# Kernel tuning notes

Hardware: AMD Instinct MI355X
Metric: run time of the kernel (lower is better)

## Reference

```python
import jax, jax.numpy as jnp
import numpy as np

B, CIN, H, W = 32, 64, 128, 128
HID, OUT, E, S, R = 64, 64, 8, 2, 16
TOP_K = 2
TEMP = 2.0
BN_EPS = 1e-5


def setup_inputs() -> dict:
    key = jax.random.key(0)
    ks = jax.random.split(key, 16)
    sc = lambda fan: 1.0 / np.sqrt(fan)
    h2 = 2 * HID
    return {
        "x": jax.random.normal(ks[0], (B, CIN, H, W), jnp.float32),
        "fe_w": jax.random.normal(ks[1], (HID, CIN), jnp.float32) * sc(CIN),
        "fe_b": jnp.zeros((HID,), jnp.float32),
        "s_w": jax.random.normal(ks[2], (S, OUT, HID), jnp.float32) * sc(HID),
        "s_b": jnp.zeros((S, OUT), jnp.float32),
        "e_w": jax.random.normal(ks[3], (E, OUT, HID), jnp.float32) * sc(HID),
        "e_b": jnp.zeros((E, OUT), jnp.float32),
        "g1_w": jax.random.normal(ks[4], (h2, HID), jnp.float32) * sc(HID),
        "g1_b": jnp.zeros((h2,), jnp.float32),
        "bn1_g": jnp.ones((h2,), jnp.float32),
        "bn1_b": jnp.zeros((h2,), jnp.float32),
        "ca1_w": jax.random.normal(ks[5], (h2 // R, h2), jnp.float32) * sc(h2),
        "ca1_b": jnp.zeros((h2 // R,), jnp.float32),
        "ca2_w": jax.random.normal(ks[6], (h2, h2 // R), jnp.float32) * sc(h2 // R),
        "ca2_b": jnp.zeros((h2,), jnp.float32),
        "g2_w": jax.random.normal(ks[7], (HID, h2), jnp.float32) * sc(h2),
        "g2_b": jnp.zeros((HID,), jnp.float32),
        "bn2_g": jnp.ones((HID,), jnp.float32),
        "bn2_b": jnp.zeros((HID,), jnp.float32),
        "g3_w": jax.random.normal(ks[8], (E, HID), jnp.float32) * sc(HID),
        "g3_b": jnp.zeros((E,), jnp.float32),
    }


def _gelu(v):
    return jax.nn.gelu(v, approximate=False)


def _bn_eval(v, g, b):
    # BatchNorm eval mode with running_mean=0, running_var=1
    return v * (g / np.sqrt(1.0 + BN_EPS)) + b


def reference(x, fe_w, fe_b, s_w, s_b, e_w, e_b, g1_w, g1_b, bn1_g, bn1_b,
              ca1_w, ca1_b, ca2_w, ca2_b, g2_w, g2_b, bn2_g, bn2_b, g3_w, g3_b):
    # feature extractor: 1x1 conv + GELU
    features = _gelu(jnp.einsum('bchw,oc->bohw', x, fe_w) + fe_b[None, :, None, None])

    # shared experts: mean of S expert outputs (sum / S)
    shared = _gelu(jnp.einsum('bchw,soc->bsohw', features, s_w)
                   + s_b[None, :, :, None, None]).mean(axis=1)

    # gating on globally pooled features [B, HID]
    gf = features.mean(axis=(2, 3))
    h1 = _gelu(_bn_eval(gf @ g1_w.T + g1_b, bn1_g, bn1_b))  # [B, 2*HID]
    # ChannelAttention on 1x1 spatial: avg_pool == max_pool == identity
    att = _gelu(h1 @ ca1_w.T + ca1_b) @ ca2_w.T + ca2_b
    h1 = h1 * jax.nn.sigmoid(att + att)  # avg_out + max_out are identical
    hh = _gelu(_bn_eval(h1 @ g2_w.T + g2_b, bn2_g, bn2_b))  # [B, HID]
    scores = hh @ g3_w.T + g3_b  # [B, E]

    top_vals, top_idx = jax.lax.top_k(scores, TOP_K)
    top_w = jax.nn.softmax(top_vals / TEMP, axis=1)  # [B, TOP_K]
    # dense per-(sample, expert) weights
    dense_w = jnp.zeros((x.shape[0], E), scores.dtype).at[
        jnp.arange(x.shape[0])[:, None], top_idx].add(top_w)

    # all experts on full batch, then weighted accumulate (matches original loop)
    eo = _gelu(jnp.einsum('bchw,eoc->beohw', features, e_w)
               + e_b[None, :, :, None, None])  # [B, E, OUT, H, W]
    routed = jnp.einsum('beohw,be->bohw', eo, dense_w)

    return shared + routed
```

## Files before the change

kernel.cpp:

```cpp
#include <hip/hip_runtime.h>
#include <hip/hip_bf16.h>
#include <stdint.h>

#define HW 16384
#define BATCH 32

typedef __bf16 bf16_t;
typedef bf16_t bf16x8 __attribute__((ext_vector_type(8)));
typedef float f32x4 __attribute__((ext_vector_type(4)));

__device__ __forceinline__ float gelu_f(float x) {
    float t = x * fmaf(x * x, 0.044715f, 1.0f);
    float e = __builtin_amdgcn_exp2f(-2.3022083f * t);
    return x * __builtin_amdgcn_rcpf(1.0f + e);
}

__device__ __forceinline__ uint32_t pk2(float a, float b) {
    union { bf16_t h[2]; uint32_t u; } z;
    z.h[0] = (bf16_t)a; z.h[1] = (bf16_t)b;
    return z.u;
}

__global__ __launch_bounds__(64)
void k0_conv(const float* __restrict__ fe_w, const float* __restrict__ s_w,
             const float* __restrict__ e_w, bf16_t* __restrict__ wbf) {
    int blk = blockIdx.x;
    int m = blk >> 3;
    int ot = (blk >> 1) & 3;
    int kh = blk & 1;
    int lane = threadIdx.x;
    int r16 = lane & 15, g = lane >> 4;

    const float* W;
    if (m == 0) W = fe_w;
    else if (m <= 2) W = s_w + (size_t)(m - 1) * 4096;
    else W = e_w + (size_t)(m - 3) * 4096;

    const float* src = W + (ot * 16 + r16) * 64 + kh * 32 + g * 8;
    float4 lo = ((const float4*)src)[0];
    float4 hi = ((const float4*)src)[1];
    bf16x8 r;
    r[0] = (bf16_t)lo.x; r[1] = (bf16_t)lo.y; r[2] = (bf16_t)lo.z; r[3] = (bf16_t)lo.w;
    r[4] = (bf16_t)hi.x; r[5] = (bf16_t)hi.y; r[6] = (bf16_t)hi.z; r[7] = (bf16_t)hi.w;
    *(bf16x8*)(wbf + (size_t)blk * 512 + lane * 8) = r;
}

__global__ __launch_bounds__(256, 4)
void k1_feat(const float* __restrict__ x, const bf16_t* __restrict__ wbf,
             const float* __restrict__ fe_b, bf16_t* __restrict__ feat,
             float* __restrict__ gf_sum) {
    __shared__ bf16_t xs[64 * 258];
    __shared__ float gf4[4][64];

    int tid = threadIdx.x;
    int lane = tid & 63;
    int wid = tid >> 6;
    int r16 = lane & 15;
    int g = lane >> 4;
    int b = blockIdx.x >> 6;
    int stripe = blockIdx.x & 63;
    int p0 = stripe * 256;

    bf16x8 A[4][2];
    f32x4 bias[4];
#pragma unroll
    for (int ot = 0; ot < 4; ++ot) {
#pragma unroll
        for (int kh = 0; kh < 2; ++kh)
            A[ot][kh] = *(const bf16x8*)(wbf + (size_t)((0 * 4 + ot) * 2 + kh) * 512 + lane * 8);
#pragma unroll
        for (int r = 0; r < 4; ++r) bias[ot][r] = fe_b[ot * 16 + g * 4 + r];
    }

    uint32_t* xsw = (uint32_t*)xs;
#pragma unroll
    for (int i = 0; i < 16; ++i) {
        int lid = i * 256 + tid;
        int c = lid >> 6;
        int pc = lid & 63;
        float4 v = ((const float4*)(x + (size_t)(b * 64 + c) * HW + p0))[pc];
        int widx = c * 129 + pc * 2;
        xsw[widx] = pk2(v.x, v.y);
        xsw[widx + 1] = pk2(v.z, v.w);
    }
    __syncthreads();

    float gfp[4][4] = {};
    bf16_t* featb = feat + (size_t)b * HW * 64;

#pragma unroll
    for (int t = 0; t < 4; ++t) {
        int pl = (wid * 4 + t) * 16 + r16;
        bf16x8 B0, B1;
#pragma unroll
        for (int j = 0; j < 8; ++j) {
            B0[j] = xs[(g * 8 + j) * 258 + pl];
            B1[j] = xs[(32 + g * 8 + j) * 258 + pl];
        }
        int pg = p0 + pl;
#pragma unroll
        for (int ot = 0; ot < 4; ++ot) {
            f32x4 y = {0.f, 0.f, 0.f, 0.f};
            y = __builtin_amdgcn_mfma_f32_16x16x32_bf16(A[ot][0], B0, y, 0, 0, 0);
            y = __builtin_amdgcn_mfma_f32_16x16x32_bf16(A[ot][1], B1, y, 0, 0, 0);
            float vr[4];
#pragma unroll
            for (int r = 0; r < 4; ++r) {
                float v = gelu_f(y[r] + bias[ot][r]);
                gfp[ot][r] += v;
                vr[r] = v;
            }
            uint2 st;
            st.x = pk2(vr[0], vr[1]);
            st.y = pk2(vr[2], vr[3]);
            *(uint2*)(featb + (size_t)pg * 64 + ot * 16 + g * 4) = st;
        }
    }

#pragma unroll
    for (int ot = 0; ot < 4; ++ot) {
#pragma unroll
        for (int r = 0; r < 4; ++r) {
            float v = gfp[ot][r];
            v += __shfl_xor(v, 1);
            v += __shfl_xor(v, 2);
            v += __shfl_xor(v, 4);
            v += __shfl_xor(v, 8);
            if (r16 == 0) gf4[wid][ot * 16 + g * 4 + r] = v;
        }
    }
    __syncthreads();
    if (tid < 64) {
        float s = gf4[0][tid] + gf4[1][tid] + gf4[2][tid] + gf4[3][tid];
        atomicAdd(gf_sum + b * 64 + tid, s);
    }
}

__global__ __launch_bounds__(256)
void k2_gate(const float* __restrict__ gf_sum,
             const float* __restrict__ g1_w, const float* __restrict__ g1_b,
             const float* __restrict__ bn1_g, const float* __restrict__ bn1_b,
             const float* __restrict__ ca1_w, const float* __restrict__ ca1_b,
             const float* __restrict__ ca2_w, const float* __restrict__ ca2_b,
             const float* __restrict__ g2_w, const float* __restrict__ g2_b,
             const float* __restrict__ bn2_g, const float* __restrict__ bn2_b,
             const float* __restrict__ g3_w, const float* __restrict__ g3_b,
             int* __restrict__ gidx, float* __restrict__ gw) {
    __shared__ float gf[32 * 64];
    __shared__ float h1[32 * 128];
    __shared__ float a1[32 * 8];
    __shared__ float hh[32 * 64];
    __shared__ float sc[32 * 8];
    const float R1 = 0.99999500003749969f;
    int tid = threadIdx.x;

    for (int i = tid; i < 2048; i += 256) gf[i] = gf_sum[i] * (1.0f / 16384.0f);
    __syncthreads();

    for (int e = tid; e < 4096; e += 256) {
        int b = e >> 7, j = e & 127;
        float s = g1_b[j];
        for (int c = 0; c < 64; ++c) s += gf[b * 64 + c] * g1_w[j * 64 + c];
        s = s * (bn1_g[j] * R1) + bn1_b[j];
        h1[e] = gelu_f(s);
    }
    __syncthreads();
    {
        int b = tid >> 3, j = tid & 7;
        float s = ca1_b[j];
        for (int c = 0; c < 128; ++c) s += h1[b * 128 + c] * ca1_w[j * 128 + c];
        a1[tid] = gelu_f(s);
    }
    __syncthreads();
    for (int e = tid; e < 4096; e += 256) {
        int b = e >> 7, j = e & 127;
        float s = ca2_b[j];
        for (int r = 0; r < 8; ++r) s += a1[b * 8 + r] * ca2_w[j * 8 + r];
        float e2 = __builtin_amdgcn_exp2f(-2.8853901f * s);
        h1[e] = h1[e] * __builtin_amdgcn_rcpf(1.0f + e2);
    }
    __syncthreads();
    for (int e = tid; e < 2048; e += 256) {
        int b = e >> 6, j = e & 63;
        float s = g2_b[j];
        for (int c = 0; c < 128; ++c) s += h1[b * 128 + c] * g2_w[j * 128 + c];
        s = s * (bn2_g[j] * R1) + bn2_b[j];
        hh[e] = gelu_f(s);
    }
    __syncthreads();
    {
        int b = tid >> 3, j = tid & 7;
        float s = g3_b[j];
        for (int c = 0; c < 64; ++c) s += hh[b * 64 + c] * g3_w[j * 64 + c];
        sc[tid] = s;
    }
    __syncthreads();
    if (tid < 32) {
        int b = tid;
        float v0 = -1e30f, v1 = -1e30f;
        int i0 = 0, i1 = 0;
        for (int e = 0; e < 8; ++e) {
            float s = sc[b * 8 + e];
            if (s > v0) { v1 = v0; i1 = i0; v0 = s; i0 = e; }
            else if (s > v1) { v1 = s; i1 = e; }
        }
        float t = __builtin_amdgcn_exp2f(0.7213475f * (v1 - v0));
        float den = __builtin_amdgcn_rcpf(1.0f + t);
        gidx[b * 2] = i0; gidx[b * 2 + 1] = i1;
        gw[b * 2] = den; gw[b * 2 + 1] = t * den;
    }
}

__global__ __launch_bounds__(256, 4)
void k3_out(const bf16_t* __restrict__ feat, const bf16_t* __restrict__ wbf,
            const float* __restrict__ s_b, const float* __restrict__ e_b,
            const int* __restrict__ gidx, const float* __restrict__ gw,
            float* __restrict__ out) {
    int tid = threadIdx.x;
    int lane = tid & 63, wid = tid >> 6;
    int r16 = lane & 15, g = lane >> 4;
    int b = blockIdx.x >> 5;
    int stripe = blockIdx.x & 31;

    int i0 = gidx[2 * b], i1 = gidx[2 * b + 1];
    float coef[4] = {0.5f, 0.5f, gw[2 * b], gw[2 * b + 1]};
    int mats[4] = {1, 2, 3 + i0, 3 + i1};
    const float* Bm[4] = {s_b, s_b + 64, e_b + i0 * 64, e_b + i1 * 64};

    bf16x8 A[4][2];
    f32x4 biasr[4];
#pragma unroll
    for (int m = 0; m < 4; ++m) {
#pragma unroll
        for (int kh = 0; kh < 2; ++kh)
            A[m][kh] = *(const bf16x8*)(wbf + (size_t)((mats[m] * 4 + wid) * 2 + kh) * 512 + lane * 8);
#pragma unroll
        for (int r = 0; r < 4; ++r) biasr[m][r] = Bm[m][wid * 16 + g * 4 + r];
    }

    const uint4* fb = (const uint4*)(feat + (size_t)b * HW * 64);
    float* outb = out + (size_t)b * 64 * HW + (size_t)(wid * 16 + g * 4) * HW;
    int pbase = stripe * 512 + r16;

#pragma unroll 2
    for (int t = 0; t < 32; ++t) {
        int p = pbase + t * 16;
        uint4 u0 = fb[p * 8 + g];
        uint4 u1 = fb[p * 8 + 4 + g];
        bf16x8 B0 = __builtin_bit_cast(bf16x8, u0);
        bf16x8 B1 = __builtin_bit_cast(bf16x8, u1);
        f32x4 acc = {0.f, 0.f, 0.f, 0.f};
#pragma unroll
        for (int m = 0; m < 4; ++m) {
            f32x4 y = {0.f, 0.f, 0.f, 0.f};
            y = __builtin_amdgcn_mfma_f32_16x16x32_bf16(A[m][0], B0, y, 0, 0, 0);
            y = __builtin_amdgcn_mfma_f32_16x16x32_bf16(A[m][1], B1, y, 0, 0, 0);
#pragma unroll
            for (int r = 0; r < 4; ++r)
                acc[r] += coef[m] * gelu_f(y[r] + biasr[m][r]);
        }
#pragma unroll
        for (int r = 0; r < 4; ++r)
            outb[(size_t)r * HW + p] = acc[r];
    }
}

extern "C" void kernel_launch(void* const* d_in, const int* in_sizes, int n_in,
                              void* d_out, int out_size, void* d_ws, size_t ws_size,
                              hipStream_t stream) {
    const float* x     = (const float*)d_in[0];
    const float* fe_w  = (const float*)d_in[1];
    const float* fe_b  = (const float*)d_in[2];
    const float* s_w   = (const float*)d_in[3];
    const float* s_b   = (const float*)d_in[4];
    const float* e_w   = (const float*)d_in[5];
    const float* e_b   = (const float*)d_in[6];
    const float* g1_w  = (const float*)d_in[7];
    const float* g1_b  = (const float*)d_in[8];
    const float* bn1_g = (const float*)d_in[9];
    const float* bn1_b = (const float*)d_in[10];
    const float* ca1_w = (const float*)d_in[11];
    const float* ca1_b = (const float*)d_in[12];
    const float* ca2_w = (const float*)d_in[13];
    const float* ca2_b = (const float*)d_in[14];
    const float* g2_w  = (const float*)d_in[15];
    const float* g2_b  = (const float*)d_in[16];
    const float* bn2_g = (const float*)d_in[17];
    const float* bn2_b = (const float*)d_in[18];
    const float* g3_w  = (const float*)d_in[19];
    const float* g3_b  = (const float*)d_in[20];
    float* out = (float*)d_out;

    char* wsb = (char*)d_ws;
    bf16_t* feat  = (bf16_t*)wsb;
    float* gf_sum = (float*)(wsb + (size_t)67108864);
    int* gidx     = (int*)(wsb + 67108864 + 8192);
    float* gwts   = (float*)(wsb + 67108864 + 8192 + 256);
    bf16_t* wbf   = (bf16_t*)(wsb + 67125248);

    hipMemsetAsync(gf_sum, 0, 32 * 64 * sizeof(float), stream);
    k0_conv<<<88, 64, 0, stream>>>(fe_w, s_w, e_w, wbf);
    k1_feat<<<2048, 256, 0, stream>>>(x, wbf, fe_b, feat, gf_sum);
    k2_gate<<<1, 256, 0, stream>>>(gf_sum, g1_w, g1_b, bn1_g, bn1_b, ca1_w, ca1_b,
                                   ca2_w, ca2_b, g2_w, g2_b, bn2_g, bn2_b, g3_w, g3_b,
                                   gidx, gwts);
    k3_out<<<1024, 256, 0, stream>>>(feat, wbf, s_b, e_b, gidx, gwts, out);
}
```

Measured before the change: 372.0 us.

## Load x via global_load_lds into swizzled LDS, halve stripes, parallelize gate per batch

k1_feat now copies fp32 x straight into LDS with direct global-to-LDS loads and an XOR swizzle, then converts to bf16 when building MFMA operands. The pixel stripe per block drops from 256 to 128, doubling the grid, which should improve latency hiding and occupancy. k2_gate becomes one block per batch sample, with the gating weights staged transposed and padded in LDS, so the serial single-block gating work is spread across 32 blocks. The cost is redundant weight staging in every gate block and fp32 LDS use for x.

```diff
diff --git a/kernel.cpp b/kernel.cpp
--- a/kernel.cpp
+++ b/kernel.cpp
@@ -19,6 +19,12 @@
     union { bf16_t h[2]; uint32_t u; } z;
     z.h[0] = (bf16_t)a; z.h[1] = (bf16_t)b;
     return z.u;
+}
+
+__device__ __forceinline__ void load16_to_lds(const float* g, float* lds) {
+    __builtin_amdgcn_global_load_lds(
+        (const __attribute__((address_space(1))) uint32_t*)g,
+        (__attribute__((address_space(3))) uint32_t*)lds, 16, 0, 0);
 }
 
 __global__ __launch_bounds__(64)
@@ -49,7 +55,7 @@
 void k1_feat(const float* __restrict__ x, const bf16_t* __restrict__ wbf,
              const float* __restrict__ fe_b, bf16_t* __restrict__ feat,
              float* __restrict__ gf_sum) {
-    __shared__ bf16_t xs[64 * 258];
+    __shared__ float xs[64 * 128];
     __shared__ float gf4[4][64];
 
     int tid = threadIdx.x;
@@ -57,9 +63,9 @@
     int wid = tid >> 6;
     int r16 = lane & 15;
     int g = lane >> 4;
-    int b = blockIdx.x >> 6;
-    int stripe = blockIdx.x & 63;
-    int p0 = stripe * 256;
+    int b = blockIdx.x >> 7;
+    int stripe = blockIdx.x & 127;
+    int p0 = stripe * 128;
 
     bf16x8 A[4][2];
     f32x4 bias[4];
@@ -67,21 +73,22 @@
     for (int ot = 0; ot < 4; ++ot) {
 #pragma unroll
         for (int kh = 0; kh < 2; ++kh)
-            A[ot][kh] = *(const bf16x8*)(wbf + (size_t)((0 * 4 + ot) * 2 + kh) * 512 + lane * 8);
+            A[ot][kh] = *(const bf16x8*)(wbf + (size_t)(ot * 2 + kh) * 512 + lane * 8);
 #pragma unroll
         for (int r = 0; r < 4; ++r) bias[ot][r] = fe_b[ot * 16 + g * 4 + r];
     }
 
-    uint32_t* xsw = (uint32_t*)xs;
-#pragma unroll
-    for (int i = 0; i < 16; ++i) {
-        int lid = i * 256 + tid;
-        int c = lid >> 6;
-        int pc = lid & 63;
-        float4 v = ((const float4*)(x + (size_t)(b * 64 + c) * HW + p0))[pc];
-        int widx = c * 129 + pc * 2;
-        xsw[widx] = pk2(v.x, v.y);
-        xsw[widx + 1] = pk2(v.z, v.w);
+    {
+        int rsub = lane >> 5;
+        int j = lane & 31;
+#pragma unroll
+        for (int s = 0; s < 8; ++s) {
+            int c = wid * 16 + s * 2 + rsub;
+            int gr = (c >> 3) & 3;
+            const float* gsrc = x + (size_t)(b * 64 + c) * HW + p0 + ((j ^ (gr << 2)) << 2);
+            float* ldst = xs + (wid * 16 + s * 2) * 128;
+            load16_to_lds(gsrc, ldst);
+        }
     }
     __syncthreads();
 
@@ -89,15 +96,16 @@
     bf16_t* featb = feat + (size_t)b * HW * 64;
 
 #pragma unroll
-    for (int t = 0; t < 4; ++t) {
-        int pl = (wid * 4 + t) * 16 + r16;
+    for (int t = 0; t < 2; ++t) {
+        int a = wid * 2 + t;
+        int wbase = 16 * (a ^ g) + r16;
         bf16x8 B0, B1;
 #pragma unroll
         for (int j = 0; j < 8; ++j) {
-            B0[j] = xs[(g * 8 + j) * 258 + pl];
-            B1[j] = xs[(32 + g * 8 + j) * 258 + pl];
-        }
-        int pg = p0 + pl;
+            B0[j] = (bf16_t)xs[(g * 8 + j) * 128 + wbase];
+            B1[j] = (bf16_t)xs[(32 + g * 8 + j) * 128 + wbase];
+        }
+        int pg = p0 + a * 16 + r16;
 #pragma unroll
         for (int ot = 0; ot < 4; ++ot) {
             f32x4 y = {0.f, 0.f, 0.f, 0.f};
@@ -146,61 +154,96 @@
              const float* __restrict__ bn2_g, const float* __restrict__ bn2_b,
              const float* __restrict__ g3_w, const float* __restrict__ g3_b,
              int* __restrict__ gidx, float* __restrict__ gw) {
-    __shared__ float gf[32 * 64];
-    __shared__ float h1[32 * 128];
-    __shared__ float a1[32 * 8];
-    __shared__ float hh[32 * 64];
-    __shared__ float sc[32 * 8];
+    __shared__ float w1t[128 * 65];
+    __shared__ float wc1[8 * 129];
+    __shared__ float wc2[128 * 9];
+    __shared__ float w2t[64 * 129];
+    __shared__ float w3[8 * 65];
+    __shared__ float gf[64], h1[128], a1[8], hh[64], sc[8];
     const float R1 = 0.99999500003749969f;
     int tid = threadIdx.x;
-
-    for (int i = tid; i < 2048; i += 256) gf[i] = gf_sum[i] * (1.0f / 16384.0f);
-    __syncthreads();
-
-    for (int e = tid; e < 4096; e += 256) {
-        int b = e >> 7, j = e & 127;
+    int b = blockIdx.x;
+
+    for (int i = tid; i < 2048; i += 256) {
+        float4 v = ((const float4*)g1_w)[i];
+        float* d = w1t + (i >> 4) * 65 + (i & 15) * 4;
+        d[0] = v.x; d[1] = v.y; d[2] = v.z; d[3] = v.w;
+    }
+    for (int i = tid; i < 2048; i += 256) {
+        float4 v = ((const float4*)g2_w)[i];
+        float* d = w2t + (i >> 5) * 129 + (i & 31) * 4;
+        d[0] = v.x; d[1] = v.y; d[2] = v.z; d[3] = v.w;
+    }
+    if (tid < 256) {
+        int i = tid;
+        float4 v = ((const float4*)ca1_w)[i];
+        float* d = wc1 + (i >> 5) * 129 + (i & 31) * 4;
+        d[0] = v.x; d[1] = v.y; d[2] = v.z; d[3] = v.w;
+    }
+    if (tid < 256) {
+        int i = tid;
+        float4 v = ((const float4*)ca2_w)[i];
+        float* d = wc2 + (i >> 1) * 9 + (i & 1) * 4;
+        d[0] = v.x; d[1] = v.y; d[2] = v.z; d[3] = v.w;
+    }
+    if (tid < 128) {
+        int i = tid;
+        float4 v = ((const float4*)g3_w)[i];
+        float* d = w3 + (i >> 4) * 65 + (i & 15) * 4;
+        d[0] = v.x; d[1] = v.y; d[2] = v.z; d[3] = v.w;
+    }
+    if (tid < 64) gf[tid] = gf_sum[b * 64 + tid] * (1.0f / 16384.0f);
+    __syncthreads();
+
+    if (tid < 128) {
+        int j = tid;
         float s = g1_b[j];
-        for (int c = 0; c < 64; ++c) s += gf[b * 64 + c] * g1_w[j * 64 + c];
+#pragma unroll 8
+        for (int c = 0; c < 64; ++c) s += gf[c] * w1t[j * 65 + c];
         s = s * (bn1_g[j] * R1) + bn1_b[j];
-        h1[e] = gelu_f(s);
-    }
-    __syncthreads();
-    {
-        int b = tid >> 3, j = tid & 7;
+        h1[j] = gelu_f(s);
+    }
+    __syncthreads();
+    if (tid < 8) {
+        int j = tid;
         float s = ca1_b[j];
-        for (int c = 0; c < 128; ++c) s += h1[b * 128 + c] * ca1_w[j * 128 + c];
-        a1[tid] = gelu_f(s);
-    }
-    __syncthreads();
-    for (int e = tid; e < 4096; e += 256) {
-        int b = e >> 7, j = e & 127;
+#pragma unroll 8
+        for (int c = 0; c < 128; ++c) s += h1[c] * wc1[j * 129 + c];
+        a1[j] = gelu_f(s);
+    }
+    __syncthreads();
+    if (tid < 128) {
+        int j = tid;
         float s = ca2_b[j];
-        for (int r = 0; r < 8; ++r) s += a1[b * 8 + r] * ca2_w[j * 8 + r];
+#pragma unroll
+        for (int r = 0; r < 8; ++r) s += a1[r] * wc2[j * 9 + r];
         float e2 = __builtin_amdgcn_exp2f(-2.8853901f * s);
-        h1[e] = h1[e] * __builtin_amdgcn_rcpf(1.0f + e2);
-    }
-    __syncthreads();
-    for (int e = tid; e < 2048; e += 256) {
-        int b = e >> 6, j = e & 63;
+        h1[j] = h1[j] * __builtin_amdgcn_rcpf(1.0f + e2);
+    }
+    __syncthreads();
+    if (tid < 64) {
+        int j = tid;
         float s = g2_b[j];
-        for (int c = 0; c < 128; ++c) s += h1[b * 128 + c] * g2_w[j * 128 + c];
+#pragma unroll 8
+        for (int c = 0; c < 128; ++c) s += h1[c] * w2t[j * 129 + c];
         s = s * (bn2_g[j] * R1) + bn2_b[j];
-        hh[e] = gelu_f(s);
-    }
-    __syncthreads();
-    {
-        int b = tid >> 3, j = tid & 7;
+        hh[j] = gelu_f(s);
+    }
+    __syncthreads();
+    if (tid < 8) {
+        int j = tid;
         float s = g3_b[j];
-        for (int c = 0; c < 64; ++c) s += hh[b * 64 + c] * g3_w[j * 64 + c];
-        sc[tid] = s;
-    }
-    __syncthreads();
-    if (tid < 32) {
-        int b = tid;
+#pragma unroll 8
+        for (int c = 0; c < 64; ++c) s += hh[c] * w3[j * 65 + c];
+        sc[j] = s;
+    }
+    __syncthreads();
+    if (tid == 0) {
         float v0 = -1e30f, v1 = -1e30f;
         int i0 = 0, i1 = 0;
+#pragma unroll
         for (int e = 0; e < 8; ++e) {
-            float s = sc[b * 8 + e];
+            float s = sc[e];
             if (s > v0) { v1 = v0; i1 = i0; v0 = s; i0 = e; }
             else if (s > v1) { v1 = s; i1 = e; }
         }
@@ -300,9 +343,9 @@
 
     hipMemsetAsync(gf_sum, 0, 32 * 64 * sizeof(float), stream);
     k0_conv<<<88, 64, 0, stream>>>(fe_w, s_w, e_w, wbf);
-    k1_feat<<<2048, 256, 0, stream>>>(x, wbf, fe_b, feat, gf_sum);
-    k2_gate<<<1, 256, 0, stream>>>(gf_sum, g1_w, g1_b, bn1_g, bn1_b, ca1_w, ca1_b,
-                                   ca2_w, ca2_b, g2_w, g2_b, bn2_g, bn2_b, g3_w, g3_b,
-                                   gidx, gwts);
+    k1_feat<<<4096, 256, 0, stream>>>(x, wbf, fe_b, feat, gf_sum);
+    k2_gate<<<32, 256, 0, stream>>>(gf_sum, g1_w, g1_b, bn1_g, bn1_b, ca1_w, ca1_b,
+                                    ca2_w, ca2_b, g2_w, g2_b, bn2_g, bn2_b, g3_w, g3_b,
+                                    gidx, gwts);
     k3_out<<<1024, 256, 0, stream>>>(feat, wbf, s_b, e_b, gidx, gwts, out);
 }
```

Result: faster. 335.8 us (-9.7%).
